# Performance work log

Measured on AMD Instinct MI355X. Metric: run time of the kernel, lower is better.

Reference implementation:

```python
import jax, jax.numpy as jnp
import numpy as np

ALPHA = 0.3      # keras LeakyReLU default
BN_EPS = 1e-3    # keras BatchNormalization default
RF, STRIDE = 8, 8


def leaky(x):
    return jnp.where(x >= 0, x, ALPHA * x)


def batchnorm(x, gamma, beta):
    # training-mode BN (train_flag=True): batch statistics over N,H,W
    mean = jnp.mean(x, axis=(0, 1, 2), keepdims=True)
    var = jnp.var(x, axis=(0, 1, 2), keepdims=True)
    return gamma * (x - mean) * jax.lax.rsqrt(var + BN_EPS) + beta


def cbl(x, W, gamma, beta):
    y = jax.lax.conv_general_dilated(x, W, (1, 1), 'SAME',
                                     dimension_numbers=('NHWC', 'HWIO', 'NHWC'))
    return leaky(batchnorm(y, gamma, beta))


def tcbl(x, W, gamma, beta):
    y = jax.lax.conv_transpose(x, W, (2, 2), 'SAME',
                               dimension_numbers=('NHWC', 'HWIO', 'NHWC'))
    return leaky(batchnorm(y, gamma, beta))


def setup_inputs() -> dict:
    key = jax.random.key(0)
    ks = jax.random.split(key, 8)
    B, H, W, C = 8, 128, 128, 128
    nH = (H - RF) // STRIDE + 1
    nW = (W - RF) // STRIDE + 1
    nWin = nH * nW  # 256
    inputs = jax.random.normal(ks[0], (B, H, W, C), dtype=jnp.float32)
    conv_scale = 1.0 / np.sqrt(3 * 3 * C)
    Wq = jax.random.normal(ks[1], (3, 3, C, 128), dtype=jnp.float32) * conv_scale
    Wk = jax.random.normal(ks[2], (3, 3, C, 128), dtype=jnp.float32) * conv_scale
    beta_bias = jax.random.normal(ks[3], (1, 1, 1, nWin), dtype=jnp.float32) * 0.05
    Wt = jax.random.normal(ks[4], (4, 4, nWin, 128), dtype=jnp.float32) / np.sqrt(4 * 4 * nWin)
    return {
        'inputs': inputs,
        'Wq': Wq, 'gq': jnp.ones((128,), jnp.float32), 'bq': jnp.zeros((128,), jnp.float32),
        'Wk': Wk, 'gk': jnp.ones((128,), jnp.float32), 'bk': jnp.zeros((128,), jnp.float32),
        'beta_bias': beta_bias,
        'g1': jnp.ones((nWin,), jnp.float32), 'b1': jnp.zeros((nWin,), jnp.float32),
        'Wt': Wt, 'gt': jnp.ones((128,), jnp.float32), 'bt': jnp.zeros((128,), jnp.float32),
    }


def reference(inputs, Wq, gq, bq, Wk, gk, bk, beta_bias, g1, b1, Wt, gt, bt):
    Q = cbl(inputs, Wq, gq, bq)   # (B,H,W,C)
    K = cbl(inputs, Wk, gk, bk)
    B, H, W, C = Q.shape
    nH = (H - RF) // STRIDE + 1
    nW = (W - RF) // STRIDE + 1
    # window start indices -> (n, RF) gather index grids
    hh = (jnp.arange(nH) * STRIDE)[:, None] + jnp.arange(RF)[None, :]
    ww = (jnp.arange(nW) * STRIDE)[:, None] + jnp.arange(RF)[None, :]

    def patches(x):
        # (B, nH, nW, RF, RF, C) -> (B, nWin, RF*RF*C)
        p = x[:, hh[:, None, :, None], ww[None, :, None, :], :]
        return p.reshape(B, nH * nW, RF * RF * C)

    Qp = patches(Q)
    Kp = patches(K)
    # sim[b, f, q] = <K window f, Q window q>; collapses the 4-nested loop
    sim = jnp.einsum('bfd,bqd->bfq', Kp, Qp).reshape(B, nH, nW, nH * nW)
    sim = sim + beta_bias
    act = leaky(batchnorm(sim, g1, b1))
    return tcbl(act, Wt, gt, bt)  # (B, 2*nH, 2*nW, 128)
```

## Files before the change

kernel.cpp:

```cpp
#include <hip/hip_runtime.h>

typedef __attribute__((ext_vector_type(8))) short bf16x8;
typedef __attribute__((ext_vector_type(8))) unsigned short u16x8;
typedef __attribute__((ext_vector_type(4))) float f32x4;

__device__ __forceinline__ unsigned short f2b(float x) {
    unsigned int u = __float_as_uint(x);
    u += 0x7FFFu + ((u >> 16) & 1u);
    return (unsigned short)(u >> 16);
}
__device__ __forceinline__ float b2f(unsigned short h) {
    return __uint_as_float(((unsigned int)h) << 16);
}
__device__ __forceinline__ float lrelu(float v) { return v >= 0.f ? v : 0.3f * v; }

#define GLL(gp, lp) __builtin_amdgcn_global_load_lds( \
    (const __attribute__((address_space(1))) unsigned int*)(gp), \
    (__attribute__((address_space(3))) unsigned int*)(lp), 16, 0, 0)


__global__ __launch_bounds__(256) void k0a_prep(
        const float* __restrict__ Wq, const float* __restrict__ Wk,
        const float* __restrict__ Wt, unsigned short* __restrict__ WqT,
        unsigned short* __restrict__ WkT, unsigned short* __restrict__ WtT,
        float* __restrict__ S) {
    int idx = blockIdx.x * 256 + threadIdx.x;
    int gs = gridDim.x * 256;
    for (int i = idx; i < 2048; i += gs) S[i] = 0.f;
    for (int i = idx; i < 147456; i += gs) {
        int tap = i >> 14, r = i & 16383, ci = r >> 7, co = r & 127;
        int ch = ci >> 6, e = ci & 63;
        int dst = ((tap * 2 + ch) * 128 + co) * 64 + (((e >> 3) ^ (co & 7)) << 3) + (e & 7);
        WqT[dst] = f2b(Wq[i]);
        WkT[dst] = f2b(Wk[i]);
    }
    for (int i = idx; i < 524288; i += gs) {
        int t = i >> 15, r = i & 32767, ci = r >> 7, co = r & 127;
        WtT[(((size_t)t << 7) + co) * 256 + ci] = f2b(Wt[i]);
    }
}

__global__ __launch_bounds__(256) void k0b_padx(const float* __restrict__ X,
                                                unsigned short* __restrict__ Xb) {
    int c = blockIdx.x * 256 + threadIdx.x;
    int k8 = c & 7;
    int t = c >> 3;
    int wp = t % 130; t /= 130;
    int ch = t & 1; t >>= 1;
    int hp = t % 130; int b = t / 130;
    u16x8 o;
    if (hp >= 1 && hp <= 128 && wp >= 1 && wp <= 128) {
        const float* s = X + (((size_t)(b * 128 + hp - 1) * 128) + (wp - 1)) * 128 + ch * 64 + k8 * 8;
        float4 f0 = *(const float4*)(s);
        float4 f1 = *(const float4*)(s + 4);
        o[0] = f2b(f0.x); o[1] = f2b(f0.y); o[2] = f2b(f0.z); o[3] = f2b(f0.w);
        o[4] = f2b(f1.x); o[5] = f2b(f1.y); o[6] = f2b(f1.z); o[7] = f2b(f1.w);
    } else {
#pragma unroll
        for (int j = 0; j < 8; ++j) o[j] = 0;
    }
    *(u16x8*)&Xb[(size_t)c * 8] = o;
}

__global__ __launch_bounds__(512, 4) void k1_conv(
        const unsigned short* __restrict__ Xb,
        const unsigned short* __restrict__ WqT, const unsigned short* __restrict__ WkT,
        unsigned short* __restrict__ Qraw, unsigned short* __restrict__ Kraw,
        float* __restrict__ S) {
    __shared__ unsigned short s_row[2 * 130 * 72];
    __shared__ unsigned short s_w[2][128 * 64];
    __shared__ float s_st[256];
    const int tid = threadIdx.x;
    const int x = blockIdx.x;
    const int xcd = x & 7, sdec = x >> 3;
    const int b = sdec >> 4, r16 = sdec & 15;
    const int hp = xcd * 8 + (r16 >> 1), conv = r16 & 1;
    const int h0 = hp * 2;
    const int lane = tid & 63, wv = tid >> 6;
    const int wm = wv & 3, wn = wv >> 2;
    const int l15 = lane & 15, kof = (lane >> 4) * 8;
    const int ar = wm >> 1;
    const int awb = (wm & 1) * 64;
    const int nb = wn * 64;

    const unsigned short* W = conv ? WkT : WqT;
    const int gofs = wv * 2048 + lane * 16;

    f32x4 acc[4][4];
#pragma unroll
    for (int i = 0; i < 4; ++i)
#pragma unroll
        for (int j = 0; j < 4; ++j) acc[i][j] = (f32x4){0.f, 0.f, 0.f, 0.f};
    if (tid < 256) s_st[tid] = 0.f;

    {
        const char* src = (const char*)W;
        char* dst = (char*)&s_w[0][0] + wv * 2048;
        GLL(src + gofs, dst);
        GLL(src + gofs + 1024, dst + 1024);
    }

#pragma unroll
    for (int ch = 0; ch < 2; ++ch) {
#pragma unroll
        for (int dy = 0; dy < 3; ++dy) {
#pragma unroll
            for (int dx = 0; dx < 3; ++dx) {
                const int p = (ch * 3 + dy) * 3 + dx;
                __builtin_amdgcn_s_barrier();
                if (dx == 0) {
                    const unsigned short* src0 = Xb + (size_t)((b * 130 + h0 + dy) * 2 + ch) * 8320;
                    const unsigned short* src1 = Xb + (size_t)((b * 130 + h0 + dy + 1) * 2 + ch) * 8320;
                    for (int c = tid; c < 2080; c += 512) {
                        int r = (c >= 1040);
                        int cw = r ? c - 1040 : c;
                        int w = cw >> 3, k8 = cw & 7;
                        *(u16x8*)&s_row[(r * 130 + w) * 72 + k8 * 8] =
                            *(const u16x8*)&((r ? src1 : src0)[cw * 8]);
                    }
                }
                if (p < 17) {
                    const int pn = p + 1;
                    const int nch = pn / 9, ntap = pn % 9;
                    const char* src = (const char*)(W + ((size_t)(ntap * 2 + nch) << 13));
                    char* dst = (char*)&s_w[pn & 1][0] + wv * 2048;
                    GLL(src + gofs, dst);
                    GLL(src + gofs + 1024, dst + 1024);
                    asm volatile("s_waitcnt vmcnt(2) lgkmcnt(0)" ::: "memory");
                } else {
                    asm volatile("s_waitcnt vmcnt(0) lgkmcnt(0)" ::: "memory");
                }
                __builtin_amdgcn_sched_barrier(0);
                __builtin_amdgcn_s_barrier();
                const unsigned short* wb = &s_w[p & 1][0];
#pragma unroll
                for (int kc = 0; kc < 2; ++kc) {
                    const int ci = kc * 32 + kof;
                    bf16x8 a[4], bb[4];
#pragma unroll
                    for (int mf = 0; mf < 4; ++mf)
                        a[mf] = *(const bf16x8*)&s_row[(ar * 130 + awb + mf * 16 + l15 + dx) * 72 + ci];
#pragma unroll
                    for (int nf = 0; nf < 4; ++nf) {
                        int co = nb + nf * 16 + l15;
                        bb[nf] = *(const bf16x8*)&wb[co * 64 + (((ci >> 3) ^ (co & 7)) << 3)];
                    }
#pragma unroll
                    for (int mf = 0; mf < 4; ++mf)
#pragma unroll
                        for (int nf = 0; nf < 4; ++nf)
                            acc[mf][nf] = __builtin_amdgcn_mfma_f32_16x16x32_bf16(
                                a[mf], bb[nf], acc[mf][nf], 0, 0, 0);
                }
            }
        }
    }
    __syncthreads();
    unsigned short* obase = conv ? Kraw : Qraw;
    const int h = h0 + ar;
    float sl[4] = {0.f, 0.f, 0.f, 0.f}, ssl[4] = {0.f, 0.f, 0.f, 0.f};
#pragma unroll
    for (int mf = 0; mf < 4; ++mf)
#pragma unroll
        for (int nf = 0; nf < 4; ++nf)
#pragma unroll
            for (int r = 0; r < 4; ++r) {
                float v = acc[mf][nf][r];
                int w = awb + mf * 16 + (lane >> 4) * 4 + r;
                int co = nb + nf * 16 + l15;
                obase[((size_t)(b * 128 + h) * 128 + w) * 128 + co] = f2b(v);
                sl[nf] += v; ssl[nf] += v * v;
            }
#pragma unroll
    for (int nf = 0; nf < 4; ++nf) {
        float s = sl[nf], ss = ssl[nf];
        s += __shfl_xor(s, 16); s += __shfl_xor(s, 32);
        ss += __shfl_xor(ss, 16); ss += __shfl_xor(ss, 32);
        if (lane < 16) {
            int chn = nb + nf * 16 + lane;
            atomicAdd(&s_st[chn], s);
            atomicAdd(&s_st[128 + chn], ss);
        }
    }
    __syncthreads();
    if (tid < 256) {
        int dst = (tid < 128) ? (conv * 128 + tid) : (256 + conv * 128 + (tid - 128));
        atomicAdd(&S[dst], s_st[tid]);
    }
}

__global__ __launch_bounds__(512, 2) void k3_sim(const unsigned short* __restrict__ Qp,
                                                 const unsigned short* __restrict__ Kp,
                                                 const float* __restrict__ S,
                                                 const float* __restrict__ gq, const float* __restrict__ bq,
                                                 const float* __restrict__ gk, const float* __restrict__ bk,
                                                 float* __restrict__ part) {
    __shared__ unsigned short sA[128 * 136];
    __shared__ unsigned short sB[128 * 136];
    __shared__ float s_p[512];
    const int tid = threadIdx.x;
    const int x = blockIdx.x;
    const int kc = x & 7, sdec = x >> 3;
    const int b = sdec >> 2, mn = sdec & 3;
    const int mi = mn >> 1, ni = mn & 1;
    const int lane = tid & 63, wv = tid >> 6;
    const int wm = wv & 1, wn = wv >> 1;
    if (tid < 256) {
        const float inv_n = 1.f / 131072.f;
        float mean = S[tid] * inv_n;
        float var = S[256 + tid] * inv_n - mean * mean;
        float g  = (tid < 128) ? gq[tid] : gk[tid - 128];
        float be = (tid < 128) ? bq[tid] : bk[tid - 128];
        float sc = g * rsqrtf(var + 1e-3f);
        s_p[tid] = sc;
        s_p[256 + tid] = be - mean * sc;
    }
    f32x4 acc[4][2];
#pragma unroll
    for (int i = 0; i < 4; ++i)
#pragma unroll
        for (int j = 0; j < 2; ++j) acc[i][j] = (f32x4){0.f, 0.f, 0.f, 0.f};
    const int kof = (lane >> 4) * 8;
    const int arow = wm * 64 + (lane & 15);
    const int brow = wn * 32 + (lane & 15);

    for (int s = 0; s < 8; ++s) {
        const int py = kc, px = s;
        __syncthreads();
        for (int c = tid; c < 2048; c += 512) {
            int r = c >> 4, k8 = c & 15;
            int cb = k8 * 8;
            int f = mi * 128 + r;
            size_t sa = ((size_t)(b * 128 + ((f >> 4) * 8 + py)) * 128 + ((f & 15) * 8 + px)) * 128 + cb;
            int q = ni * 128 + r;
            size_t sb = ((size_t)(b * 128 + ((q >> 4) * 8 + py)) * 128 + ((q & 15) * 8 + px)) * 128 + cb;
            u16x8 va = *(const u16x8*)&Kp[sa];
            u16x8 vb = *(const u16x8*)&Qp[sb];
            u16x8 oa, ob;
#pragma unroll
            for (int j = 0; j < 8; ++j) {
                float fk = b2f(va[j]);
                fk = lrelu(s_p[128 + cb + j] * fk + s_p[384 + cb + j]);
                oa[j] = f2b(fk);
                float fq = b2f(vb[j]);
                fq = lrelu(s_p[cb + j] * fq + s_p[256 + cb + j]);
                ob[j] = f2b(fq);
            }
            *(u16x8*)&sA[r * 136 + cb] = oa;
            *(u16x8*)&sB[r * 136 + cb] = ob;
        }
        __syncthreads();
#pragma unroll
        for (int k4 = 0; k4 < 4; ++k4) {
            const int ci = k4 * 32 + kof;
            bf16x8 a[4], bb[2];
#pragma unroll
            for (int mf = 0; mf < 4; ++mf)
                a[mf] = *(const bf16x8*)&sA[(arow + mf * 16) * 136 + ci];
#pragma unroll
            for (int nf = 0; nf < 2; ++nf)
                bb[nf] = *(const bf16x8*)&sB[(brow + nf * 16) * 136 + ci];
#pragma unroll
            for (int mf = 0; mf < 4; ++mf)
#pragma unroll
                for (int nf = 0; nf < 2; ++nf)
                    acc[mf][nf] = __builtin_amdgcn_mfma_f32_16x16x32_bf16(
                        a[mf], bb[nf], acc[mf][nf], 0, 0, 0);
        }
    }
    const size_t base = (size_t)(kc * 8 + b) * 65536;
#pragma unroll
    for (int mf = 0; mf < 4; ++mf)
#pragma unroll
        for (int nf = 0; nf < 2; ++nf)
#pragma unroll
            for (int r = 0; r < 4; ++r) {
                int f = mi * 128 + wm * 64 + mf * 16 + (lane >> 4) * 4 + r;
                int q = ni * 128 + wn * 32 + nf * 16 + (lane & 15);
                part[base + (size_t)f * 256 + q] = acc[mf][nf][r];
            }
}

__global__ __launch_bounds__(256) void k4_red(const float* __restrict__ part,
                                              const float* __restrict__ beta,
                                              float* __restrict__ sim, float* __restrict__ S) {
    int row0 = blockIdx.x * 8;
    int q = threadIdx.x;
    float bsum = 0.f, bss = 0.f;
    float bb = beta[q];
    for (int rr = 0; rr < 8; ++rr) {
        int row = row0 + rr;
        float s = 0.f;
#pragma unroll
        for (int kcc = 0; kcc < 8; ++kcc)
            s += part[(size_t)kcc * 524288 + (size_t)row * 256 + q];
        s += bb;
        sim[(size_t)row * 256 + q] = s;
        bsum += s; bss += s * s;
    }
    atomicAdd(&S[512 + q], bsum);
    atomicAdd(&S[768 + q], bss);
}

__global__ __launch_bounds__(256) void k5b_act(const float* __restrict__ sim,
                                               const float* __restrict__ S,
                                               const float* __restrict__ g1, const float* __restrict__ b1,
                                               unsigned short* __restrict__ actp) {
    __shared__ float s_p[512];
    {
        int c = threadIdx.x;
        const float inv_n = 1.f / 2048.f;
        float mean = S[512 + c] * inv_n;
        float var = S[768 + c] * inv_n - mean * mean;
        float sc = g1[c] * rsqrtf(var + 1e-3f);
        s_p[c] = sc;
        s_p[256 + c] = b1[c] - mean * sc;
    }
    __syncthreads();
    int c = blockIdx.x * 256 + threadIdx.x;
    if (c >= 186624) return;
    int k8 = c & 31;
    int t = c >> 5;
    int jp = t % 18; t /= 18;
    int ip = t % 18; int b = t / 18;
    u16x8 o;
    if (ip >= 1 && ip <= 16 && jp >= 1 && jp <= 16) {
        int f = (ip - 1) * 16 + (jp - 1);
        const float* s = sim + (size_t)(b * 256 + f) * 256 + k8 * 8;
#pragma unroll
        for (int j = 0; j < 8; ++j) {
            int ci = k8 * 8 + j;
            o[j] = f2b(lrelu(s_p[ci] * s[j] + s_p[256 + ci]));
        }
    } else {
#pragma unroll
        for (int j = 0; j < 8; ++j) o[j] = 0;
    }
    *(u16x8*)&actp[(size_t)c * 8] = o;
}

__global__ __launch_bounds__(512, 2) void k6_tconv(const unsigned short* __restrict__ actp,
                                                   const unsigned short* __restrict__ WtT,
                                                   float* __restrict__ y, float* __restrict__ S) {
    __shared__ unsigned short sA[64 * 264];
    __shared__ unsigned short sB[128 * 264];
    const int tid = threadIdx.x;
    const int x = blockIdx.x;
    const int iq = x & 3, pw = (x >> 2) & 1, ph = (x >> 3) & 1, b = x >> 4;
    const int lane = tid & 63, wv = tid >> 6;
    f32x4 acc[4];
#pragma unroll
    for (int i = 0; i < 4; ++i) acc[i] = (f32x4){0.f, 0.f, 0.f, 0.f};
    const int kof = (lane >> 4) * 8;
    const int arow = lane & 15;
    const int bco = wv * 16 + (lane & 15);

    for (int a2 = 0; a2 < 2; ++a2)
        for (int c2 = 0; c2 < 2; ++c2) {
            const int kh = ph + 2 * a2, kw = pw + 2 * c2;
            __syncthreads();
            for (int c = tid; c < 2048; c += 512) {
                int r = c >> 5, k8 = c & 31;
                int i = iq * 4 + (r >> 4), j = r & 15;
                size_t sa = (size_t)((b * 18 + (i + a2 + ph)) * 18 + (j + c2 + pw)) * 256 + k8 * 8;
                *(u16x8*)&sA[r * 264 + k8 * 8] = *(const u16x8*)&actp[sa];
            }
            for (int c = tid; c < 4096; c += 512) {
                int co = c >> 5, k8 = c & 31;
                size_t sb = (size_t)((kh * 4 + kw) * 128 + co) * 256 + k8 * 8;
                *(u16x8*)&sB[co * 264 + k8 * 8] = *(const u16x8*)&WtT[sb];
            }
            __syncthreads();
#pragma unroll
            for (int k8c = 0; k8c < 8; ++k8c) {
                const int ci = k8c * 32 + kof;
                bf16x8 bb = *(const bf16x8*)&sB[bco * 264 + ci];
#pragma unroll
                for (int mf = 0; mf < 4; ++mf) {
                    bf16x8 a = *(const bf16x8*)&sA[(arow + mf * 16) * 264 + ci];
                    acc[mf] = __builtin_amdgcn_mfma_f32_16x16x32_bf16(a, bb, acc[mf], 0, 0, 0);
                }
            }
        }
    float sl = 0.f, ssl = 0.f;
#pragma unroll
    for (int mf = 0; mf < 4; ++mf)
#pragma unroll
        for (int r = 0; r < 4; ++r) {
            float v = acc[mf][r];
            int m = mf * 16 + (lane >> 4) * 4 + r;
            int i = iq * 4 + (m >> 4), j = m & 15;
            int oh = 2 * i + ph, ow = 2 * j + pw;
            y[(size_t)((b * 32 + oh) * 32 + ow) * 128 + bco] = v;
            sl += v; ssl += v * v;
        }
    sl += __shfl_xor(sl, 16); sl += __shfl_xor(sl, 32);
    ssl += __shfl_xor(ssl, 16); ssl += __shfl_xor(ssl, 32);
    if (lane < 16) {
        atomicAdd(&S[1024 + wv * 16 + lane], sl);
        atomicAdd(&S[1152 + wv * 16 + lane], ssl);
    }
}

__global__ __launch_bounds__(256) void k8_out(const float* __restrict__ y,
                                              const float* __restrict__ S,
                                              const float* __restrict__ gt, const float* __restrict__ bt,
                                              float* __restrict__ out) {
    __shared__ float s_p[256];
    if (threadIdx.x < 128) {
        int c = threadIdx.x;
        const float inv_n = 1.f / 8192.f;
        float mean = S[1024 + c] * inv_n;
        float var = S[1152 + c] * inv_n - mean * mean;
        float sc = gt[c] * rsqrtf(var + 1e-3f);
        s_p[c] = sc;
        s_p[128 + c] = bt[c] - mean * sc;
    }
    __syncthreads();
    int c = blockIdx.x * 256 + threadIdx.x;
    const float4 v = *(const float4*)&y[(size_t)c * 4];
    int cb = (c & 31) * 4;
    float4 o;
    o.x = lrelu(s_p[cb + 0] * v.x + s_p[128 + cb + 0]);
    o.y = lrelu(s_p[cb + 1] * v.y + s_p[128 + cb + 1]);
    o.z = lrelu(s_p[cb + 2] * v.z + s_p[128 + cb + 2]);
    o.w = lrelu(s_p[cb + 3] * v.w + s_p[128 + cb + 3]);
    *(float4*)&out[(size_t)c * 4] = o;
}

extern "C" void kernel_launch(void* const* d_in, const int* in_sizes, int n_in,
                              void* d_out, int out_size, void* d_ws, size_t ws_size,
                              hipStream_t stream) {
    (void)in_sizes; (void)n_in; (void)out_size; (void)ws_size;
    const float* X    = (const float*)d_in[0];
    const float* Wq   = (const float*)d_in[1];
    const float* gq   = (const float*)d_in[2];
    const float* bq   = (const float*)d_in[3];
    const float* Wk   = (const float*)d_in[4];
    const float* gk   = (const float*)d_in[5];
    const float* bk   = (const float*)d_in[6];
    const float* beta = (const float*)d_in[7];
    const float* g1   = (const float*)d_in[8];
    const float* b1   = (const float*)d_in[9];
    const float* Wt   = (const float*)d_in[10];
    const float* gt   = (const float*)d_in[11];
    const float* bt   = (const float*)d_in[12];

    char* ws = (char*)d_ws;
    unsigned short* Qraw = (unsigned short*)(ws + 0ull);
    unsigned short* Kraw = (unsigned short*)(ws + 33554432ull);
    unsigned short* WqT  = (unsigned short*)(ws + 67108864ull);
    unsigned short* WkT  = (unsigned short*)(ws + 67403776ull);
    unsigned short* WtT  = (unsigned short*)(ws + 67698688ull);
    float* S             = (float*)(ws + 68747264ull);
    unsigned short* Xb   = (unsigned short*)(ws + 68761600ull);
    float* part          = (float*)(ws + 68761600ull);
    float* sim           = (float*)(ws + 0ull);
    unsigned short* actp = (unsigned short*)(ws + 4194304ull);
    float* y             = (float*)(ws + 8388608ull);
    float* out           = (float*)d_out;

    k0a_prep<<<1024, 256, 0, stream>>>(Wq, Wk, Wt, WqT, WkT, WtT, S);
    k0b_padx<<<8450, 256, 0, stream>>>(X, Xb);
    k1_conv<<<1024, 512, 0, stream>>>(Xb, WqT, WkT, Qraw, Kraw, S);
    k3_sim<<<256, 512, 0, stream>>>(Qraw, Kraw, S, gq, bq, gk, bk, part);
    k4_red<<<256, 256, 0, stream>>>(part, beta, sim, S);
    k5b_act<<<729, 256, 0, stream>>>(sim, S, g1, b1, actp);
    k6_tconv<<<128, 512, 0, stream>>>(actp, WtT, y, S);
    k8_out<<<1024, 256, 0, stream>>>(y, S, gt, bt, out);
}
```

Measured before the change: 170.4 us.

## Fuse input padding/bf16 conversion into conv kernel and retile conv and tconv

```diff
diff --git a/kernel.cpp b/kernel.cpp
--- a/kernel.cpp
+++ b/kernel.cpp
@@ -40,30 +40,8 @@
     }
 }
 
-__global__ __launch_bounds__(256) void k0b_padx(const float* __restrict__ X,
-                                                unsigned short* __restrict__ Xb) {
-    int c = blockIdx.x * 256 + threadIdx.x;
-    int k8 = c & 7;
-    int t = c >> 3;
-    int wp = t % 130; t /= 130;
-    int ch = t & 1; t >>= 1;
-    int hp = t % 130; int b = t / 130;
-    u16x8 o;
-    if (hp >= 1 && hp <= 128 && wp >= 1 && wp <= 128) {
-        const float* s = X + (((size_t)(b * 128 + hp - 1) * 128) + (wp - 1)) * 128 + ch * 64 + k8 * 8;
-        float4 f0 = *(const float4*)(s);
-        float4 f1 = *(const float4*)(s + 4);
-        o[0] = f2b(f0.x); o[1] = f2b(f0.y); o[2] = f2b(f0.z); o[3] = f2b(f0.w);
-        o[4] = f2b(f1.x); o[5] = f2b(f1.y); o[6] = f2b(f1.z); o[7] = f2b(f1.w);
-    } else {
-#pragma unroll
-        for (int j = 0; j < 8; ++j) o[j] = 0;
-    }
-    *(u16x8*)&Xb[(size_t)c * 8] = o;
-}
-
-__global__ __launch_bounds__(512, 4) void k1_conv(
-        const unsigned short* __restrict__ Xb,
+__global__ __launch_bounds__(256, 2) void k1_conv(
+        const float* __restrict__ X,
         const unsigned short* __restrict__ WqT, const unsigned short* __restrict__ WkT,
         unsigned short* __restrict__ Qraw, unsigned short* __restrict__ Kraw,
         float* __restrict__ S) {
@@ -77,56 +55,66 @@
     const int hp = xcd * 8 + (r16 >> 1), conv = r16 & 1;
     const int h0 = hp * 2;
     const int lane = tid & 63, wv = tid >> 6;
-    const int wm = wv & 3, wn = wv >> 2;
+    const int wm = wv & 1, wn = wv >> 1;
     const int l15 = lane & 15, kof = (lane >> 4) * 8;
-    const int ar = wm >> 1;
-    const int awb = (wm & 1) * 64;
     const int nb = wn * 64;
 
     const unsigned short* W = conv ? WkT : WqT;
-    const int gofs = wv * 2048 + lane * 16;
-
-    f32x4 acc[4][4];
-#pragma unroll
-    for (int i = 0; i < 4; ++i)
+    const int gofs = wv * 4096 + lane * 16;
+
+    f32x4 acc[8][4];
+#pragma unroll
+    for (int i = 0; i < 8; ++i)
 #pragma unroll
         for (int j = 0; j < 4; ++j) acc[i][j] = (f32x4){0.f, 0.f, 0.f, 0.f};
-    if (tid < 256) s_st[tid] = 0.f;
+    s_st[tid] = 0.f;
 
     {
         const char* src = (const char*)W;
-        char* dst = (char*)&s_w[0][0] + wv * 2048;
+        char* dst = (char*)&s_w[0][0] + wv * 4096;
         GLL(src + gofs, dst);
         GLL(src + gofs + 1024, dst + 1024);
-    }
-
-#pragma unroll
+        GLL(src + gofs + 2048, dst + 2048);
+        GLL(src + gofs + 3072, dst + 3072);
+    }
+
     for (int ch = 0; ch < 2; ++ch) {
-#pragma unroll
         for (int dy = 0; dy < 3; ++dy) {
 #pragma unroll
             for (int dx = 0; dx < 3; ++dx) {
                 const int p = (ch * 3 + dy) * 3 + dx;
                 __builtin_amdgcn_s_barrier();
                 if (dx == 0) {
-                    const unsigned short* src0 = Xb + (size_t)((b * 130 + h0 + dy) * 2 + ch) * 8320;
-                    const unsigned short* src1 = Xb + (size_t)((b * 130 + h0 + dy + 1) * 2 + ch) * 8320;
-                    for (int c = tid; c < 2080; c += 512) {
+                    for (int c = tid; c < 2080; c += 256) {
                         int r = (c >= 1040);
-                        int cw = r ? c - 1040 : c;
+                        int cw = c - r * 1040;
                         int w = cw >> 3, k8 = cw & 7;
-                        *(u16x8*)&s_row[(r * 130 + w) * 72 + k8 * 8] =
-                            *(const u16x8*)&((r ? src1 : src0)[cw * 8]);
+                        int xh = h0 + dy + r - 1;
+                        u16x8 o;
+                        if (xh >= 0 && xh < 128 && w >= 1 && w <= 128) {
+                            const float* s = X + (((size_t)(b * 128 + xh) * 128) + (w - 1)) * 128
+                                             + ch * 64 + k8 * 8;
+                            float4 f0 = *(const float4*)(s);
+                            float4 f1 = *(const float4*)(s + 4);
+                            o[0] = f2b(f0.x); o[1] = f2b(f0.y); o[2] = f2b(f0.z); o[3] = f2b(f0.w);
+                            o[4] = f2b(f1.x); o[5] = f2b(f1.y); o[6] = f2b(f1.z); o[7] = f2b(f1.w);
+                        } else {
+#pragma unroll
+                            for (int j = 0; j < 8; ++j) o[j] = 0;
+                        }
+                        *(u16x8*)&s_row[(r * 130 + w) * 72 + k8 * 8] = o;
                     }
                 }
                 if (p < 17) {
                     const int pn = p + 1;
                     const int nch = pn / 9, ntap = pn % 9;
                     const char* src = (const char*)(W + ((size_t)(ntap * 2 + nch) << 13));
-                    char* dst = (char*)&s_w[pn & 1][0] + wv * 2048;
+                    char* dst = (char*)&s_w[pn & 1][0] + wv * 4096;
                     GLL(src + gofs, dst);
                     GLL(src + gofs + 1024, dst + 1024);
-                    asm volatile("s_waitcnt vmcnt(2) lgkmcnt(0)" ::: "memory");
+                    GLL(src + gofs + 2048, dst + 2048);
+                    GLL(src + gofs + 3072, dst + 3072);
+                    asm volatile("s_waitcnt vmcnt(4) lgkmcnt(0)" ::: "memory");
                 } else {
                     asm volatile("s_waitcnt vmcnt(0) lgkmcnt(0)" ::: "memory");
                 }
@@ -136,37 +124,39 @@
 #pragma unroll
                 for (int kc = 0; kc < 2; ++kc) {
                     const int ci = kc * 32 + kof;
-                    bf16x8 a[4], bb[4];
-#pragma unroll
-                    for (int mf = 0; mf < 4; ++mf)
-                        a[mf] = *(const bf16x8*)&s_row[(ar * 130 + awb + mf * 16 + l15 + dx) * 72 + ci];
+                    bf16x8 a[8], bb[4];
+#pragma unroll
+                    for (int mf = 0; mf < 8; ++mf)
+                        a[mf] = *(const bf16x8*)&s_row[(wm * 130 + mf * 16 + l15 + dx) * 72 + ci];
 #pragma unroll
                     for (int nf = 0; nf < 4; ++nf) {
                         int co = nb + nf * 16 + l15;
                         bb[nf] = *(const bf16x8*)&wb[co * 64 + (((ci >> 3) ^ (co & 7)) << 3)];
                     }
-#pragma unroll
-                    for (int mf = 0; mf < 4; ++mf)
+                    __builtin_amdgcn_s_setprio(1);
+#pragma unroll
+                    for (int mf = 0; mf < 8; ++mf)
 #pragma unroll
                         for (int nf = 0; nf < 4; ++nf)
                             acc[mf][nf] = __builtin_amdgcn_mfma_f32_16x16x32_bf16(
                                 a[mf], bb[nf], acc[mf][nf], 0, 0, 0);
+                    __builtin_amdgcn_s_setprio(0);
                 }
             }
         }
     }
     __syncthreads();
     unsigned short* obase = conv ? Kraw : Qraw;
-    const int h = h0 + ar;
+    const int h = h0 + wm;
     float sl[4] = {0.f, 0.f, 0.f, 0.f}, ssl[4] = {0.f, 0.f, 0.f, 0.f};
 #pragma unroll
-    for (int mf = 0; mf < 4; ++mf)
+    for (int mf = 0; mf < 8; ++mf)
 #pragma unroll
         for (int nf = 0; nf < 4; ++nf)
 #pragma unroll
             for (int r = 0; r < 4; ++r) {
                 float v = acc[mf][nf][r];
-                int w = awb + mf * 16 + (lane >> 4) * 4 + r;
+                int w = mf * 16 + (lane >> 4) * 4 + r;
                 int co = nb + nf * 16 + l15;
                 obase[((size_t)(b * 128 + h) * 128 + w) * 128 + co] = f2b(v);
                 sl[nf] += v; ssl[nf] += v * v;
@@ -183,7 +173,7 @@
         }
     }
     __syncthreads();
-    if (tid < 256) {
+    {
         int dst = (tid < 128) ? (conv * 128 + tid) : (256 + conv * 128 + (tid - 128));
         atomicAdd(&S[dst], s_st[tid]);
     }
@@ -342,15 +332,15 @@
 __global__ __launch_bounds__(512, 2) void k6_tconv(const unsigned short* __restrict__ actp,
                                                    const unsigned short* __restrict__ WtT,
                                                    float* __restrict__ y, float* __restrict__ S) {
-    __shared__ unsigned short sA[64 * 264];
+    __shared__ unsigned short sA[32 * 264];
     __shared__ unsigned short sB[128 * 264];
     const int tid = threadIdx.x;
     const int x = blockIdx.x;
-    const int iq = x & 3, pw = (x >> 2) & 1, ph = (x >> 3) & 1, b = x >> 4;
+    const int iq = x & 7, pw = (x >> 3) & 1, ph = (x >> 4) & 1, b = x >> 5;
     const int lane = tid & 63, wv = tid >> 6;
-    f32x4 acc[4];
-#pragma unroll
-    for (int i = 0; i < 4; ++i) acc[i] = (f32x4){0.f, 0.f, 0.f, 0.f};
+    f32x4 acc[2];
+#pragma unroll
+    for (int i = 0; i < 2; ++i) acc[i] = (f32x4){0.f, 0.f, 0.f, 0.f};
     const int kof = (lane >> 4) * 8;
     const int arow = lane & 15;
     const int bco = wv * 16 + (lane & 15);
@@ -359,9 +349,9 @@
         for (int c2 = 0; c2 < 2; ++c2) {
             const int kh = ph + 2 * a2, kw = pw + 2 * c2;
             __syncthreads();
-            for (int c = tid; c < 2048; c += 512) {
+            for (int c = tid; c < 1024; c += 512) {
                 int r = c >> 5, k8 = c & 31;
-                int i = iq * 4 + (r >> 4), j = r & 15;
+                int i = iq * 2 + (r >> 4), j = r & 15;
                 size_t sa = (size_t)((b * 18 + (i + a2 + ph)) * 18 + (j + c2 + pw)) * 256 + k8 * 8;
                 *(u16x8*)&sA[r * 264 + k8 * 8] = *(const u16x8*)&actp[sa];
             }
@@ -376,7 +366,7 @@
                 const int ci = k8c * 32 + kof;
                 bf16x8 bb = *(const bf16x8*)&sB[bco * 264 + ci];
 #pragma unroll
-                for (int mf = 0; mf < 4; ++mf) {
+                for (int mf = 0; mf < 2; ++mf) {
                     bf16x8 a = *(const bf16x8*)&sA[(arow + mf * 16) * 264 + ci];
                     acc[mf] = __builtin_amdgcn_mfma_f32_16x16x32_bf16(a, bb, acc[mf], 0, 0, 0);
                 }
@@ -384,12 +374,12 @@
         }
     float sl = 0.f, ssl = 0.f;
 #pragma unroll
-    for (int mf = 0; mf < 4; ++mf)
+    for (int mf = 0; mf < 2; ++mf)
 #pragma unroll
         for (int r = 0; r < 4; ++r) {
             float v = acc[mf][r];
             int m = mf * 16 + (lane >> 4) * 4 + r;
-            int i = iq * 4 + (m >> 4), j = m & 15;
+            int i = iq * 2 + (m >> 4), j = m & 15;
             int oh = 2 * i + ph, ow = 2 * j + pw;
             y[(size_t)((b * 32 + oh) * 32 + ow) * 128 + bco] = v;
             sl += v; ssl += v * v;
@@ -453,7 +443,6 @@
     unsigned short* WkT  = (unsigned short*)(ws + 67403776ull);
     unsigned short* WtT  = (unsigned short*)(ws + 67698688ull);
     float* S             = (float*)(ws + 68747264ull);
-    unsigned short* Xb   = (unsigned short*)(ws + 68761600ull);
     float* part          = (float*)(ws + 68761600ull);
     float* sim           = (float*)(ws + 0ull);
     unsigned short* actp = (unsigned short*)(ws + 4194304ull);
@@ -461,11 +450,10 @@
     float* out           = (float*)d_out;
 
     k0a_prep<<<1024, 256, 0, stream>>>(Wq, Wk, Wt, WqT, WkT, WtT, S);
-    k0b_padx<<<8450, 256, 0, stream>>>(X, Xb);
-    k1_conv<<<1024, 512, 0, stream>>>(Xb, WqT, WkT, Qraw, Kraw, S);
+    k1_conv<<<1024, 256, 0, stream>>>(X, WqT, WkT, Qraw, Kraw, S);
     k3_sim<<<256, 512, 0, stream>>>(Qraw, Kraw, S, gq, bq, gk, bk, part);
     k4_red<<<256, 256, 0, stream>>>(part, beta, sim, S);
     k5b_act<<<729, 256, 0, stream>>>(sim, S, g1, b1, actp);
-    k6_tconv<<<128, 512, 0, stream>>>(actp, WtT, y, S);
+    k6_tconv<<<256, 512, 0, stream>>>(actp, WtT, y, S);
     k8_out<<<1024, 256, 0, stream>>>(y, S, gt, bt, out);
 }
```

Result: slower. 174.8 us (+2.6%).
